# Kernel optimization log

Measured on AMD Instinct MI355X. Metric: run time of the kernel, lower is better.

Reference implementation:

```python
import jax, jax.numpy as jnp
import numpy as np

IN_CH, PATCH, STRIDE, RES, NCLS = 3, 64, 32, 4096, 1000
SPECTRAL_RADIUS = 0.9


def setup_inputs() -> dict:
    key = jax.random.key(0)
    ks = jax.random.split(key, 8)
    x = jax.random.normal(ks[0], (128, IN_CH, 8224), dtype=jnp.float32)
    # Conv1d weights: [out=PATCH, in=IN_CH, k=PATCH]
    fan_in = IN_CH * PATCH
    bound = 1.0 / np.sqrt(fan_in)
    conv_w = jax.random.uniform(ks[1], (PATCH, IN_CH, PATCH), minval=-bound, maxval=bound, dtype=jnp.float32)
    conv_b = jax.random.uniform(ks[2], (PATCH,), minval=-bound, maxval=bound, dtype=jnp.float32)
    # Reservoir weights (uniform(-0.5, 0.5)), spectral-radius normalized
    rng = np.random.default_rng(0)
    Wres = rng.random((RES, RES), dtype=np.float32) - 0.5
    max_eig = np.max(np.abs(np.linalg.eigvals(Wres)))
    Wres = Wres * (SPECTRAL_RADIUS / max_eig)
    W_reservoir = jnp.asarray(Wres, dtype=jnp.float32)
    W_input = jax.random.uniform(ks[3], (RES, PATCH), minval=-0.5, maxval=0.5, dtype=jnp.float32)
    # cls/dist tokens init to zeros (as in torch)
    cls_token = jnp.zeros((1, PATCH), dtype=jnp.float32)
    dist_token = jnp.zeros((1, PATCH), dtype=jnp.float32)
    hb = 1.0 / np.sqrt(RES)
    w_cls = jax.random.uniform(ks[4], (NCLS, RES), minval=-hb, maxval=hb, dtype=jnp.float32)
    b_cls = jax.random.uniform(ks[5], (NCLS,), minval=-hb, maxval=hb, dtype=jnp.float32)
    w_dist = jax.random.uniform(ks[6], (NCLS, RES), minval=-hb, maxval=hb, dtype=jnp.float32)
    b_dist = jax.random.uniform(ks[7], (NCLS,), minval=-hb, maxval=hb, dtype=jnp.float32)
    return {"x": x, "conv_w": conv_w, "conv_b": conv_b, "W_reservoir": W_reservoir,
            "W_input": W_input, "cls_token": cls_token, "dist_token": dist_token,
            "w_cls": w_cls, "b_cls": b_cls, "w_dist": w_dist, "b_dist": b_dist}


def reference(x, conv_w, conv_b, W_reservoir, W_input, cls_token, dist_token,
              w_cls, b_cls, w_dist, b_dist):
    B = x.shape[0]
    # PatchEmbed: conv1d -> [B, PATCH, L]
    feat = jax.lax.conv_general_dilated(
        x, conv_w, window_strides=(STRIDE,), padding='VALID',
        dimension_numbers=('NCH', 'OIH', 'NCH')) + conv_b[None, :, None]
    WinT = W_input.T  # [PATCH, RES]
    us = jnp.transpose(feat, (2, 0, 1))  # [L, B, PATCH]
    h0 = jnp.zeros((B, RES), dtype=x.dtype)

    def step(h, u):
        h = jnp.tanh(h @ W_reservoir + u @ WinT)
        return h, None

    h, _ = jax.lax.scan(step, h0, us)
    cls_tok = jnp.broadcast_to(cls_token, (B, PATCH))
    dist_tok = jnp.broadcast_to(dist_token, (B, PATCH))
    h_cls = jnp.tanh(h @ W_reservoir + cls_tok @ WinT)
    h_dist = jnp.tanh(h @ W_reservoir + dist_tok @ WinT)
    cls_out = h_cls @ w_cls.T + b_cls
    dist_out = h_dist @ w_dist.T + b_dist
    # eval mode: log_softmax of the averaged logits
    return jax.nn.log_softmax((cls_out + dist_out) * 0.5, axis=1)
```

## Files before the change

### kernel.cpp

```cpp
#include <hip/hip_runtime.h>
#include <hip/hip_bf16.h>

#define LSTEPS 256

typedef short  bf16x8_t  __attribute__((ext_vector_type(8)));
typedef float  f32x4_t   __attribute__((ext_vector_type(4)));
typedef unsigned short us4_t __attribute__((ext_vector_type(4)));

static __device__ __forceinline__ unsigned short f2bf(float f) {
  unsigned int u = __float_as_uint(f);
  unsigned int r = (u + 0x7fffu + ((u >> 16) & 1u)) >> 16;
  return (unsigned short)r;
}
static __device__ __forceinline__ float tanh_fast(float x) {
  float e = __expf(2.f * x);
  return 1.f - 2.f / (e + 1.f);
}

__global__ __launch_bounds__(256) void prep_wc_kernel(
    const float* __restrict__ wcls, const float* __restrict__ wdist,
    unsigned short* __restrict__ Wcat)
{
  const int row = blockIdx.x;
  const float* src = nullptr;
  if (row < 1000) src = wcls + (size_t)row * 4096;
  else if (row >= 1024 && row < 2024) src = wdist + (size_t)(row - 1024) * 4096;
  unsigned short* dst = Wcat + (size_t)row * 4096;
  #pragma unroll 4
  for (int r = 0; r < 16; ++r) {
    const int c = r * 256 + threadIdx.x;
    dst[c] = src ? f2bf(src[c]) : (unsigned short)0;
  }
}

__global__ __launch_bounds__(256) void conv_kernel(
    const float* __restrict__ x, const float* __restrict__ w,
    const float* __restrict__ bias, unsigned short* __restrict__ U)
{
  __shared__ float wl[192][64];
  const int b  = blockIdx.x >> 4;
  const int tg = blockIdx.x & 15;
  const int tid = threadIdx.x;
  for (int i = tid; i < 64 * 192; i += 256)
    wl[i % 192][i / 192] = w[i];
  __syncthreads();
  const int wv = tid >> 6, p = tid & 63;
  const float* xb = x + (size_t)b * (3 * 8224);
  const float bp = bias[p];
  for (int tt = 0; tt < 4; ++tt) {
    const int t = tg * 16 + wv * 4 + tt;
    float acc = bp;
    const float* xw = xb + t * 32;
    #pragma unroll
    for (int c = 0; c < 3; ++c)
      #pragma unroll 8
      for (int k = 0; k < 64; ++k)
        acc += xw[c * 8224 + k] * wl[c * 64 + k][p];
    U[((size_t)t * 8 + (p >> 3)) * 1024 + (size_t)b * 8 + (p & 7)] = f2bf(acc);
  }
}

__global__ __launch_bounds__(256) void prep_tok_kernel(
    const float* __restrict__ cls, const float* __restrict__ dist,
    unsigned short* __restrict__ U)
{
  const int i = blockIdx.x * 256 + threadIdx.x;
  const int s = i >> 13, rem = i & 8191;
  const int kg = rem >> 10, e = rem & 7;
  const float* tok = s ? dist : cls;
  U[(size_t)(256 + s) * 8192 + rem] = f2bf(tok[kg * 8 + e]);
}

__global__ __launch_bounds__(512, 2) void reservoir_persistent(
    const float* __restrict__ wres,
    const unsigned short* __restrict__ U,
    const float* __restrict__ winp,
    unsigned short* __restrict__ A0, unsigned short* __restrict__ A1,
    unsigned short* __restrict__ Hcls, unsigned short* __restrict__ Hdist,
    unsigned int* __restrict__ lcnt, unsigned int* __restrict__ gcnt,
    unsigned int* __restrict__ lgo)
{
  extern __shared__ char smem[];
  float* Pl = (float*)smem;
  unsigned short* Wu = (unsigned short*)(smem + 67584);

  const int bid  = blockIdx.x;
  const int tid  = threadIdx.x;
  const int w    = tid >> 6;
  const int lane = tid & 63;
  const int q    = lane >> 4;
  const int r    = lane & 15;
  const int cg   = bid >> 1;
  const int bh   = bid & 1;
  const int nbase = cg * 32;
  const int grp  = bid & 7;

  bf16x8_t wf[16][2];
  #pragma unroll
  for (int kk = 0; kk < 16; ++kk)
    #pragma unroll
    for (int ct = 0; ct < 2; ++ct) {
      const float* src = wres + (size_t)(w * 512 + kk * 32 + q * 8) * 4096
                              + nbase + ct * 16 + r;
      bf16x8_t f;
      #pragma unroll
      for (int e = 0; e < 8; ++e) f[e] = (short)f2bf(src[(size_t)e * 4096]);
      wf[kk][ct] = f;
    }
  if (w < 2) {
    #pragma unroll
    for (int ct = 0; ct < 2; ++ct) {
      const float* src = winp + (size_t)(nbase + ct * 16 + r) * 64 + w * 32 + q * 8;
      bf16x8_t f;
      #pragma unroll
      for (int e = 0; e < 8; ++e) f[e] = (short)f2bf(src[e]);
      *(bf16x8_t*)(Wu + ((size_t)(ct * 2 + w) * 64 + lane) * 8) = f;
    }
  }

  const int au = (w * 64 + q) * 128 + bh * 64 + r;
  const int uu = (w * 4 + q) * 128 + bh * 64 + r;

  const int erow = tid >> 3;
  const int cb   = (tid & 7) * 4;
  const size_t awoff = ((size_t)(cg * 4 + (cb >> 3)) * 128 + bh * 64 + erow) * 8 + (cb & 7);
  const size_t hoff  = (size_t)(bh * 64 + erow) * 4096 + nbase + cb;

  unsigned int phase = 0;

#define LD(BUF, KK)                                                          \
  { BUF[0] = Ab[au + (KK) * 512];      BUF[1] = Ab[au + (KK) * 512 + 16];    \
    BUF[2] = Ab[au + (KK) * 512 + 32]; BUF[3] = Ab[au + (KK) * 512 + 48]; }

#define MMc(BUF, KK)                                                         \
  { acc[0][0] = __builtin_amdgcn_mfma_f32_16x16x32_bf16(BUF[0], wf[KK][0], acc[0][0], 0, 0, 0); \
    acc[0][1] = __builtin_amdgcn_mfma_f32_16x16x32_bf16(BUF[0], wf[KK][1], acc[0][1], 0, 0, 0); \
    acc[1][0] = __builtin_amdgcn_mfma_f32_16x16x32_bf16(BUF[1], wf[KK][0], acc[1][0], 0, 0, 0); \
    acc[1][1] = __builtin_amdgcn_mfma_f32_16x16x32_bf16(BUF[1], wf[KK][1], acc[1][1], 0, 0, 0); \
    acc[2][0] = __builtin_amdgcn_mfma_f32_16x16x32_bf16(BUF[2], wf[KK][0], acc[2][0], 0, 0, 0); \
    acc[2][1] = __builtin_amdgcn_mfma_f32_16x16x32_bf16(BUF[2], wf[KK][1], acc[2][1], 0, 0, 0); \
    acc[3][0] = __builtin_amdgcn_mfma_f32_16x16x32_bf16(BUF[3], wf[KK][0], acc[3][0], 0, 0, 0); \
    acc[3][1] = __builtin_amdgcn_mfma_f32_16x16x32_bf16(BUF[3], wf[KK][1], acc[3][1], 0, 0, 0); }

#define MMU(BUF, WU0, WU1)                                                   \
  { acc[0][0] = __builtin_amdgcn_mfma_f32_16x16x32_bf16(BUF[0], WU0, acc[0][0], 0, 0, 0); \
    acc[0][1] = __builtin_amdgcn_mfma_f32_16x16x32_bf16(BUF[0], WU1, acc[0][1], 0, 0, 0); \
    acc[1][0] = __builtin_amdgcn_mfma_f32_16x16x32_bf16(BUF[1], WU0, acc[1][0], 0, 0, 0); \
    acc[1][1] = __builtin_amdgcn_mfma_f32_16x16x32_bf16(BUF[1], WU1, acc[1][1], 0, 0, 0); \
    acc[2][0] = __builtin_amdgcn_mfma_f32_16x16x32_bf16(BUF[2], WU0, acc[2][0], 0, 0, 0); \
    acc[2][1] = __builtin_amdgcn_mfma_f32_16x16x32_bf16(BUF[2], WU1, acc[2][1], 0, 0, 0); \
    acc[3][0] = __builtin_amdgcn_mfma_f32_16x16x32_bf16(BUF[3], WU0, acc[3][0], 0, 0, 0); \
    acc[3][1] = __builtin_amdgcn_mfma_f32_16x16x32_bf16(BUF[3], WU1, acc[3][1], 0, 0, 0); }

  #pragma unroll 1
  for (int t = 0; t < LSTEPS + 2; ++t) {
    const unsigned short* Arp = (t <= LSTEPS) ? ((t & 1) ? A1 : A0) : A0;
    unsigned short* Awp = ((t + 1) & 1) ? A1 : A0;
    const bf16x8_t* __restrict__ Ab = (const bf16x8_t*)Arp;
    const bf16x8_t* __restrict__ Ub = (const bf16x8_t*)(U + (size_t)t * 8192);

    f32x4_t acc[4][2];
    #pragma unroll
    for (int m = 0; m < 4; ++m) {
      acc[m][0] = (f32x4_t){0.f, 0.f, 0.f, 0.f};
      acc[m][1] = (f32x4_t){0.f, 0.f, 0.f, 0.f};
    }

    bf16x8_t b0[4], b1[4];
    LD(b0, 0); LD(b1, 1);

    MMc(b0, 0);  LD(b0, 2);
    MMc(b1, 1);  LD(b1, 3);
    MMc(b0, 2);  LD(b0, 4);
    MMc(b1, 3);  LD(b1, 5);
    MMc(b0, 4);  LD(b0, 6);
    MMc(b1, 5);  LD(b1, 7);
    MMc(b0, 6);  LD(b0, 8);
    MMc(b1, 7);  LD(b1, 9);
    MMc(b0, 8);  LD(b0, 10);
    MMc(b1, 9);  LD(b1, 11);
    MMc(b0, 10); LD(b0, 12);
    MMc(b1, 11); LD(b1, 13);
    MMc(b0, 12); LD(b0, 14);
    MMc(b1, 13); LD(b1, 15);
    MMc(b0, 14);
    if (w < 2) {
      bf16x8_t bu[4];
      bu[0] = Ub[uu];      bu[1] = Ub[uu + 16];
      bu[2] = Ub[uu + 32]; bu[3] = Ub[uu + 48];
      MMc(b1, 15);
      bf16x8_t wu0 = *(const bf16x8_t*)(Wu + ((size_t)(0 * 2 + w) * 64 + lane) * 8);
      bf16x8_t wu1 = *(const bf16x8_t*)(Wu + ((size_t)(1 * 2 + w) * 64 + lane) * 8);
      MMU(bu, wu0, wu1);
    } else {
      MMc(b1, 15);
    }

    #pragma unroll
    for (int rt = 0; rt < 4; ++rt)
      #pragma unroll
      for (int ct = 0; ct < 2; ++ct)
        #pragma unroll
        for (int i = 0; i < 4; ++i)
          Pl[(w * 64 + rt * 16 + q * 4 + i) * 33 + ct * 16 + r] = acc[rt][ct][i];
    __syncthreads();

    {
      float s0 = 0.f, s1 = 0.f, s2 = 0.f, s3 = 0.f;
      #pragma unroll
      for (int wv = 0; wv < 8; ++wv) {
        const float* p = Pl + (wv * 64 + erow) * 33 + cb;
        s0 += p[0]; s1 += p[1]; s2 += p[2]; s3 += p[3];
      }
      us4_t o;
      o[0] = f2bf(tanh_fast(s0));
      o[1] = f2bf(tanh_fast(s1));
      o[2] = f2bf(tanh_fast(s2));
      o[3] = f2bf(tanh_fast(s3));
      if (t < LSTEPS) {
        *(us4_t*)(Awp + awoff) = o;
      } else {
        unsigned short* H = (t == LSTEPS) ? Hcls : Hdist;
        *(us4_t*)(H + hoff) = o;
      }
    }

    phase += 1;
    __syncthreads();
    if (tid == 0) {
      unsigned int prev = __hip_atomic_fetch_add(&lcnt[grp * 32], 1u,
                            __ATOMIC_RELAXED, __HIP_MEMORY_SCOPE_AGENT);
      if (prev == phase * 32u - 1u) {
        __hip_atomic_fetch_add(gcnt, 1u, __ATOMIC_RELEASE, __HIP_MEMORY_SCOPE_AGENT);
        while (__hip_atomic_load(gcnt, __ATOMIC_RELAXED, __HIP_MEMORY_SCOPE_SYSTEM)
               < phase * 8u)
          __builtin_amdgcn_s_sleep(1);
        (void)__hip_atomic_load(gcnt, __ATOMIC_ACQUIRE, __HIP_MEMORY_SCOPE_AGENT);
        __hip_atomic_store(&lgo[grp * 32], phase,
                           __ATOMIC_RELAXED, __HIP_MEMORY_SCOPE_AGENT);
      } else {
        while (__hip_atomic_load(&lgo[grp * 32], __ATOMIC_RELAXED,
                                 __HIP_MEMORY_SCOPE_SYSTEM) < phase)
          __builtin_amdgcn_s_sleep(1);
      }
    }
    __syncthreads();
  }
#undef LD
#undef MMc
#undef MMU
}

__global__ __launch_bounds__(256) void gemm_ksplit(
    const unsigned short* __restrict__ A0, const unsigned short* __restrict__ A1,
    int nsplit, int lda,
    const unsigned short* __restrict__ BT, int ldb,
    float* __restrict__ P, int ntiles, int klen, int klen_last)
{
  __shared__ unsigned short sA[128 * 64];
  __shared__ unsigned short sB[128 * 64];

  const int bid = blockIdx.x;
  const int nt = bid % ntiles;
  const int s  = bid / ntiles;
  const unsigned short* __restrict__ A = (nt < nsplit) ? A0 : A1;
  const int kb0 = s * klen;
  const int KL  = (s == 7) ? klen_last : klen;
  const int nbase = nt * 128;

  const int tid = threadIdx.x;
  const int w = tid >> 6;
  const int lane = tid & 63;
  const int wr = w >> 1, wc = w & 1;

  f32x4_t acc[4][4];
  #pragma unroll
  for (int m = 0; m < 4; ++m)
    #pragma unroll
    for (int n = 0; n < 4; ++n)
      acc[m][n] = (f32x4_t){0.f, 0.f, 0.f, 0.f};

  const int srow = lane >> 3;
  const int slotL = (lane & 7) ^ srow;

  for (int kb = 0; kb < KL; kb += 64) {
    const int kcol = kb0 + kb + slotL * 8;
    #pragma unroll
    for (int qq = 0; qq < 4; ++qq) {
      const int row = 32 * w + 8 * qq + srow;
      __builtin_amdgcn_global_load_lds(
          (const __attribute__((address_space(1))) void*)(A + (size_t)row * lda + kcol),
          (__attribute__((address_space(3))) void*)(&sA[(32 * w + 8 * qq) * 64]),
          16, 0, 0);
      __builtin_amdgcn_global_load_lds(
          (const __attribute__((address_space(1))) void*)(BT + (size_t)(nbase + row) * ldb + kcol),
          (__attribute__((address_space(3))) void*)(&sB[(32 * w + 8 * qq) * 64]),
          16, 0, 0);
    }
    __syncthreads();

    #pragma unroll
    for (int ksub = 0; ksub < 2; ++ksub) {
      bf16x8_t af[4], bfr[4];
      #pragma unroll
      for (int m = 0; m < 4; ++m) {
        const int row = 64 * wr + 16 * m + (lane & 15);
        const int kslot = (ksub * 4 + (lane >> 4)) ^ (row & 7);
        af[m] = *(const bf16x8_t*)(&sA[row * 64 + kslot * 8]);
      }
      #pragma unroll
      for (int n = 0; n < 4; ++n) {
        const int row = 64 * wc + 16 * n + (lane & 15);
        const int kslot = (ksub * 4 + (lane >> 4)) ^ (row & 7);
        bfr[n] = *(const bf16x8_t*)(&sB[row * 64 + kslot * 8]);
      }
      #pragma unroll
      for (int m = 0; m < 4; ++m)
        #pragma unroll
        for (int n = 0; n < 4; ++n)
          acc[m][n] = __builtin_amdgcn_mfma_f32_16x16x32_bf16(af[m], bfr[n], acc[m][n], 0, 0, 0);
    }
    __syncthreads();
  }

  float* __restrict__ Pp = P + (size_t)s * (128 * 4096);
  #pragma unroll
  for (int m = 0; m < 4; ++m) {
    const int rbase = 64 * wr + 16 * m + ((lane >> 4) << 2);
    #pragma unroll
    for (int n = 0; n < 4; ++n) {
      const int col = nbase + 64 * wc + 16 * n + (lane & 15);
      #pragma unroll
      for (int r = 0; r < 4; ++r)
        Pp[(size_t)(rbase + r) * 4096 + col] = acc[m][n][r];
    }
  }
}

__global__ __launch_bounds__(256) void reduce_linear_kernel(
    const float* __restrict__ P, float* __restrict__ logits)
{
  const int e = blockIdx.x * 1024 + threadIdx.x * 4;
  const int b = e >> 11;
  const int n = e & 2047;
  const size_t off = (size_t)b * 4096 + n;
  float4 sum = *(const float4*)(&P[off]);
  #pragma unroll
  for (int s = 1; s < 8; ++s) {
    float4 v = *(const float4*)(&P[(size_t)s * 524288 + off]);
    sum.x += v.x; sum.y += v.y; sum.z += v.z; sum.w += v.w;
  }
  *(float4*)(&logits[e]) = sum;
}

__global__ __launch_bounds__(256) void logsoftmax_kernel(
    const float* __restrict__ logits, const float* __restrict__ bcls,
    const float* __restrict__ bdist, float* __restrict__ out)
{
  __shared__ float v[1000];
  __shared__ float red[256];
  const int b = blockIdx.x;
  const int tid = threadIdx.x;
  float lmax = -1e30f;
  for (int n = tid; n < 1000; n += 256) {
    float val = 0.5f * (logits[(size_t)b * 2048 + n] + bcls[n]
                      + logits[(size_t)b * 2048 + 1024 + n] + bdist[n]);
    v[n] = val;
    lmax = fmaxf(lmax, val);
  }
  red[tid] = lmax; __syncthreads();
  for (int st = 128; st > 0; st >>= 1) {
    if (tid < st) red[tid] = fmaxf(red[tid], red[tid + st]);
    __syncthreads();
  }
  const float mx = red[0];
  __syncthreads();
  float lsum = 0.f;
  for (int n = tid; n < 1000; n += 256) lsum += expf(v[n] - mx);
  red[tid] = lsum; __syncthreads();
  for (int st = 128; st > 0; st >>= 1) {
    if (tid < st) red[tid] += red[tid + st];
    __syncthreads();
  }
  const float lse = logf(red[0]) + mx;
  for (int n = tid; n < 1000; n += 256) out[(size_t)b * 1000 + n] = v[n] - lse;
}

extern "C" void kernel_launch(void* const* d_in, const int* in_sizes, int n_in,
                              void* d_out, int out_size, void* d_ws, size_t ws_size,
                              hipStream_t stream)
{
  (void)in_sizes; (void)n_in; (void)out_size; (void)ws_size;
  const float* x      = (const float*)d_in[0];
  const float* convw  = (const float*)d_in[1];
  const float* convb  = (const float*)d_in[2];
  const float* wres   = (const float*)d_in[3];
  const float* winp   = (const float*)d_in[4];
  const float* clstok = (const float*)d_in[5];
  const float* dsttok = (const float*)d_in[6];
  const float* wcls   = (const float*)d_in[7];
  const float* bcls   = (const float*)d_in[8];
  const float* wdist  = (const float*)d_in[9];
  const float* bdist  = (const float*)d_in[10];
  float* out = (float*)d_out;

  char* ws = (char*)d_ws;
  unsigned short* U     = (unsigned short*)(ws + 0);
  unsigned short* A0    = (unsigned short*)(ws + 4227072);
  unsigned short* A1    = (unsigned short*)(ws + 5275648);
  unsigned short* Hcls  = (unsigned short*)(ws + 6324224);
  unsigned short* Hdist = (unsigned short*)(ws + 7372800);
  unsigned short* Wcat  = (unsigned short*)(ws + 8421376);
  float*          P     = (float*)(ws + 25198592);
  float*          logit = (float*)(ws + 41975808);
  unsigned int*   lcnt  = (unsigned int*)(ws + 43024384);
  unsigned int*   lgo   = (unsigned int*)(ws + 43025408);
  unsigned int*   gcnt  = (unsigned int*)(ws + 43026432);

  hipFuncSetAttribute((const void*)reservoir_persistent,
                      hipFuncAttributeMaxDynamicSharedMemorySize, 71680);

  hipMemsetAsync(A0, 0, 2 * 1048576, stream);
  hipMemsetAsync(lcnt, 0, 4096, stream);

  prep_wc_kernel<<<2048, 256, 0, stream>>>(wcls, wdist, Wcat);
  conv_kernel<<<2048, 256, 0, stream>>>(x, convw, convb, U);
  prep_tok_kernel<<<64, 256, 0, stream>>>(clstok, dsttok, U);

  reservoir_persistent<<<256, 512, 71680, stream>>>(
      wres, U, winp, A0, A1, Hcls, Hdist, lcnt, gcnt, lgo);

  gemm_ksplit<<<128, 256, 0, stream>>>(Hcls, Hdist, 8, 4096, Wcat, 4096, P, 16, 512, 512);
  reduce_linear_kernel<<<256, 256, 0, stream>>>(P, logit);
  logsoftmax_kernel<<<128, 256, 0, stream>>>(logit, bcls, bdist, out);
}
```

Before: 3.142 ms.

## Stream reservoir state through LDS with async global_load_lds pipeline

Replaces the direct global-to-register loads of the previous hidden state with global_load_lds DMA into a per-wave 4-slot LDS ring. Manual vmcnt waits keep several chunks in flight ahead of the MFMAs, and a __syncthreads now separates the pipeline from the partial-sum scratch. The aim is to hide global latency inside the latency-bound serial scan and to free VGPRs. In exchange, dynamic LDS grows to about 132KB, which may prevent 2 blocks per CU even though all 256 persistent blocks must be co-resident for the grid barrier. The extra LDS round-trip and barrier also add per-step overhead.

```diff
diff --git a/kernel.cpp b/kernel.cpp
--- a/kernel.cpp
+++ b/kernel.cpp
@@ -82,7 +82,7 @@
 {
   extern __shared__ char smem[];
   float* Pl = (float*)smem;
-  unsigned short* Wu = (unsigned short*)(smem + 67584);
+  unsigned short* Wu = (unsigned short*)(smem + 131072);
 
   const int bid  = blockIdx.x;
   const int tid  = threadIdx.x;
@@ -120,6 +120,8 @@
 
   const int au = (w * 64 + q) * 128 + bh * 64 + r;
   const int uu = (w * 4 + q) * 128 + bh * 64 + r;
+  char* slotw = smem + (size_t)w * 16384;
+  const int l16 = lane * 16;
 
   const int erow = tid >> 3;
   const int cb   = (tid & 7) * 4;
@@ -128,36 +130,54 @@
 
   unsigned int phase = 0;
 
-#define LD(BUF, KK)                                                          \
-  { BUF[0] = Ab[au + (KK) * 512];      BUF[1] = Ab[au + (KK) * 512 + 16];    \
-    BUF[2] = Ab[au + (KK) * 512 + 32]; BUF[3] = Ab[au + (KK) * 512 + 48]; }
-
-#define MMc(BUF, KK)                                                         \
-  { acc[0][0] = __builtin_amdgcn_mfma_f32_16x16x32_bf16(BUF[0], wf[KK][0], acc[0][0], 0, 0, 0); \
-    acc[0][1] = __builtin_amdgcn_mfma_f32_16x16x32_bf16(BUF[0], wf[KK][1], acc[0][1], 0, 0, 0); \
-    acc[1][0] = __builtin_amdgcn_mfma_f32_16x16x32_bf16(BUF[1], wf[KK][0], acc[1][0], 0, 0, 0); \
-    acc[1][1] = __builtin_amdgcn_mfma_f32_16x16x32_bf16(BUF[1], wf[KK][1], acc[1][1], 0, 0, 0); \
-    acc[2][0] = __builtin_amdgcn_mfma_f32_16x16x32_bf16(BUF[2], wf[KK][0], acc[2][0], 0, 0, 0); \
-    acc[2][1] = __builtin_amdgcn_mfma_f32_16x16x32_bf16(BUF[2], wf[KK][1], acc[2][1], 0, 0, 0); \
-    acc[3][0] = __builtin_amdgcn_mfma_f32_16x16x32_bf16(BUF[3], wf[KK][0], acc[3][0], 0, 0, 0); \
-    acc[3][1] = __builtin_amdgcn_mfma_f32_16x16x32_bf16(BUF[3], wf[KK][1], acc[3][1], 0, 0, 0); }
-
-#define MMU(BUF, WU0, WU1)                                                   \
-  { acc[0][0] = __builtin_amdgcn_mfma_f32_16x16x32_bf16(BUF[0], WU0, acc[0][0], 0, 0, 0); \
-    acc[0][1] = __builtin_amdgcn_mfma_f32_16x16x32_bf16(BUF[0], WU1, acc[0][1], 0, 0, 0); \
-    acc[1][0] = __builtin_amdgcn_mfma_f32_16x16x32_bf16(BUF[1], WU0, acc[1][0], 0, 0, 0); \
-    acc[1][1] = __builtin_amdgcn_mfma_f32_16x16x32_bf16(BUF[1], WU1, acc[1][1], 0, 0, 0); \
-    acc[2][0] = __builtin_amdgcn_mfma_f32_16x16x32_bf16(BUF[2], WU0, acc[2][0], 0, 0, 0); \
-    acc[2][1] = __builtin_amdgcn_mfma_f32_16x16x32_bf16(BUF[2], WU1, acc[2][1], 0, 0, 0); \
-    acc[3][0] = __builtin_amdgcn_mfma_f32_16x16x32_bf16(BUF[3], WU0, acc[3][0], 0, 0, 0); \
-    acc[3][1] = __builtin_amdgcn_mfma_f32_16x16x32_bf16(BUF[3], WU1, acc[3][1], 0, 0, 0); }
+#define GLLA(KK, J)                                                          \
+  __builtin_amdgcn_global_load_lds(                                          \
+      (const __attribute__((address_space(1))) void*)(Arp + (size_t)(au + (KK) * 512 + (J) * 16) * 8), \
+      (__attribute__((address_space(3))) void*)(slotw + (((KK) & 3) * 4096) + (J) * 1024), \
+      16, 0, 0)
+
+#define GLLU(J)                                                              \
+  __builtin_amdgcn_global_load_lds(                                          \
+      (const __attribute__((address_space(1))) void*)(Up + (size_t)(uu + (J) * 16) * 8), \
+      (__attribute__((address_space(3))) void*)(slotw + (J) * 1024),         \
+      16, 0, 0)
+
+#define ISSUE4A(KK)                                                          \
+  { asm volatile("s_waitcnt lgkmcnt(0)" ::: "memory");                       \
+    __builtin_amdgcn_sched_barrier(0);                                       \
+    GLLA(KK, 0); GLLA(KK, 1); GLLA(KK, 2); GLLA(KK, 3); }
+
+#define ISSUE4U()                                                            \
+  { asm volatile("s_waitcnt lgkmcnt(0)" ::: "memory");                       \
+    __builtin_amdgcn_sched_barrier(0);                                       \
+    GLLU(0); GLLU(1); GLLU(2); GLLU(3); }
+
+#define MFMA8(W0, W1)                                                        \
+    acc[0][0] = __builtin_amdgcn_mfma_f32_16x16x32_bf16(B0_, W0, acc[0][0], 0, 0, 0); \
+    acc[0][1] = __builtin_amdgcn_mfma_f32_16x16x32_bf16(B0_, W1, acc[0][1], 0, 0, 0); \
+    acc[1][0] = __builtin_amdgcn_mfma_f32_16x16x32_bf16(B1_, W0, acc[1][0], 0, 0, 0); \
+    acc[1][1] = __builtin_amdgcn_mfma_f32_16x16x32_bf16(B1_, W1, acc[1][1], 0, 0, 0); \
+    acc[2][0] = __builtin_amdgcn_mfma_f32_16x16x32_bf16(B2_, W0, acc[2][0], 0, 0, 0); \
+    acc[2][1] = __builtin_amdgcn_mfma_f32_16x16x32_bf16(B2_, W1, acc[2][1], 0, 0, 0); \
+    acc[3][0] = __builtin_amdgcn_mfma_f32_16x16x32_bf16(B3_, W0, acc[3][0], 0, 0, 0); \
+    acc[3][1] = __builtin_amdgcn_mfma_f32_16x16x32_bf16(B3_, W1, acc[3][1], 0, 0, 0)
+
+#define CHUNK(KK, VN, ISS)                                                   \
+  { const char* sp_ = slotw + (((KK) & 3) * 4096);                           \
+    asm volatile("s_waitcnt vmcnt(" #VN ")" ::: "memory");                   \
+    __builtin_amdgcn_sched_barrier(0);                                       \
+    bf16x8_t B0_ = *(const bf16x8_t*)(sp_ + l16);                            \
+    bf16x8_t B1_ = *(const bf16x8_t*)(sp_ + 1024 + l16);                     \
+    bf16x8_t B2_ = *(const bf16x8_t*)(sp_ + 2048 + l16);                     \
+    bf16x8_t B3_ = *(const bf16x8_t*)(sp_ + 3072 + l16);                     \
+    ISS;                                                                     \
+    MFMA8(wf[KK][0], wf[KK][1]); }
 
   #pragma unroll 1
   for (int t = 0; t < LSTEPS + 2; ++t) {
     const unsigned short* Arp = (t <= LSTEPS) ? ((t & 1) ? A1 : A0) : A0;
     unsigned short* Awp = ((t + 1) & 1) ? A1 : A0;
-    const bf16x8_t* __restrict__ Ab = (const bf16x8_t*)Arp;
-    const bf16x8_t* __restrict__ Ub = (const bf16x8_t*)(U + (size_t)t * 8192);
+    const unsigned short* Up = U + (size_t)t * 8192;
 
     f32x4_t acc[4][2];
     #pragma unroll
@@ -166,35 +186,41 @@
       acc[m][1] = (f32x4_t){0.f, 0.f, 0.f, 0.f};
     }
 
-    bf16x8_t b0[4], b1[4];
-    LD(b0, 0); LD(b1, 1);
-
-    MMc(b0, 0);  LD(b0, 2);
-    MMc(b1, 1);  LD(b1, 3);
-    MMc(b0, 2);  LD(b0, 4);
-    MMc(b1, 3);  LD(b1, 5);
-    MMc(b0, 4);  LD(b0, 6);
-    MMc(b1, 5);  LD(b1, 7);
-    MMc(b0, 6);  LD(b0, 8);
-    MMc(b1, 7);  LD(b1, 9);
-    MMc(b0, 8);  LD(b0, 10);
-    MMc(b1, 9);  LD(b1, 11);
-    MMc(b0, 10); LD(b0, 12);
-    MMc(b1, 11); LD(b1, 13);
-    MMc(b0, 12); LD(b0, 14);
-    MMc(b1, 13); LD(b1, 15);
-    MMc(b0, 14);
+    ISSUE4A(0); ISSUE4A(1); ISSUE4A(2); ISSUE4A(3);
+
     if (w < 2) {
-      bf16x8_t bu[4];
-      bu[0] = Ub[uu];      bu[1] = Ub[uu + 16];
-      bu[2] = Ub[uu + 32]; bu[3] = Ub[uu + 48];
-      MMc(b1, 15);
-      bf16x8_t wu0 = *(const bf16x8_t*)(Wu + ((size_t)(0 * 2 + w) * 64 + lane) * 8);
-      bf16x8_t wu1 = *(const bf16x8_t*)(Wu + ((size_t)(1 * 2 + w) * 64 + lane) * 8);
-      MMU(bu, wu0, wu1);
+      CHUNK(0, 12, ISSUE4A(4));   CHUNK(1, 12, ISSUE4A(5));
+      CHUNK(2, 12, ISSUE4A(6));   CHUNK(3, 12, ISSUE4A(7));
+      CHUNK(4, 12, ISSUE4A(8));   CHUNK(5, 12, ISSUE4A(9));
+      CHUNK(6, 12, ISSUE4A(10));  CHUNK(7, 12, ISSUE4A(11));
+      CHUNK(8, 12, ISSUE4A(12));  CHUNK(9, 12, ISSUE4A(13));
+      CHUNK(10, 12, ISSUE4A(14)); CHUNK(11, 12, ISSUE4A(15));
+      CHUNK(12, 12, ISSUE4U());
+      CHUNK(13, 12, (void)0); CHUNK(14, 8, (void)0); CHUNK(15, 4, (void)0);
+      {
+        const char* sp_ = slotw;
+        asm volatile("s_waitcnt vmcnt(0)" ::: "memory");
+        __builtin_amdgcn_sched_barrier(0);
+        bf16x8_t B0_ = *(const bf16x8_t*)(sp_ + l16);
+        bf16x8_t B1_ = *(const bf16x8_t*)(sp_ + 1024 + l16);
+        bf16x8_t B2_ = *(const bf16x8_t*)(sp_ + 2048 + l16);
+        bf16x8_t B3_ = *(const bf16x8_t*)(sp_ + 3072 + l16);
+        bf16x8_t wu0 = *(const bf16x8_t*)(Wu + ((size_t)(0 * 2 + w) * 64 + lane) * 8);
+        bf16x8_t wu1 = *(const bf16x8_t*)(Wu + ((size_t)(1 * 2 + w) * 64 + lane) * 8);
+        MFMA8(wu0, wu1);
+      }
     } else {
-      MMc(b1, 15);
-    }
+      CHUNK(0, 12, ISSUE4A(4));   CHUNK(1, 12, ISSUE4A(5));
+      CHUNK(2, 12, ISSUE4A(6));   CHUNK(3, 12, ISSUE4A(7));
+      CHUNK(4, 12, ISSUE4A(8));   CHUNK(5, 12, ISSUE4A(9));
+      CHUNK(6, 12, ISSUE4A(10));  CHUNK(7, 12, ISSUE4A(11));
+      CHUNK(8, 12, ISSUE4A(12));  CHUNK(9, 12, ISSUE4A(13));
+      CHUNK(10, 12, ISSUE4A(14)); CHUNK(11, 12, ISSUE4A(15));
+      CHUNK(12, 12, (void)0); CHUNK(13, 8, (void)0);
+      CHUNK(14, 4, (void)0);  CHUNK(15, 0, (void)0);
+    }
+
+    __syncthreads();
 
     #pragma unroll
     for (int rt = 0; rt < 4; ++rt)
@@ -246,9 +272,12 @@
     }
     __syncthreads();
   }
-#undef LD
-#undef MMc
-#undef MMU
+#undef GLLA
+#undef GLLU
+#undef ISSUE4A
+#undef ISSUE4U
+#undef MFMA8
+#undef CHUNK
 }
 
 __global__ __launch_bounds__(256) void gemm_ksplit(
@@ -418,7 +447,7 @@
   unsigned int*   gcnt  = (unsigned int*)(ws + 43026432);
 
   hipFuncSetAttribute((const void*)reservoir_persistent,
-                      hipFuncAttributeMaxDynamicSharedMemorySize, 71680);
+                      hipFuncAttributeMaxDynamicSharedMemorySize, 135168);
 
   hipMemsetAsync(A0, 0, 2 * 1048576, stream);
   hipMemsetAsync(lcnt, 0, 4096, stream);
@@ -427,7 +456,7 @@
   conv_kernel<<<2048, 256, 0, stream>>>(x, convw, convb, U);
   prep_tok_kernel<<<64, 256, 0, stream>>>(clstok, dsttok, U);
 
-  reservoir_persistent<<<256, 512, 71680, stream>>>(
+  reservoir_persistent<<<256, 512, 135168, stream>>>(
       wres, U, winp, A0, A1, Hcls, Hdist, lcnt, gcnt, lgo);
 
   gemm_ksplit<<<128, 256, 0, stream>>>(Hcls, Hdist, 8, 4096, Wcat, 4096, P, 16, 512, 512);
```

After: 8.021 ms. 155% more time.
